# Kernel tuning notes

Measured on AMD Instinct MI355X. Metric: run time of the kernel, lower is better.

Reference implementation:

```python
import jax, jax.numpy as jnp
from jax import lax
import numpy as np

N_QUBITS = 8
Q_DEPTH = 10
DIM = 256  # 2**8

# basis-state bit table; wire 0 = most-significant bit (PennyLane convention)
_bits = ((np.arange(DIM)[:, None] >> (N_QUBITS - 1 - np.arange(N_QUBITS))) & 1)
# phase layer: S on even wires (phase i), T on odd wires (phase e^{i pi/4})
_ph = np.where(np.arange(N_QUBITS) % 2 == 0, 1j, np.exp(1j * np.pi / 4))
_diag = np.prod(np.power(_ph[None, :], _bits), axis=1)
# entangling_layer_3 CZ pattern
_cz = np.ones(DIM)
for i, j in [(0, 1), (2, 3), (4, 5), (6, 7), (1, 2), (3, 4), (5, 6)]:
    _cz = _cz * ((-1.0) ** (_bits[:, i] * _bits[:, j]))
DIAG = jnp.asarray((_diag * _cz).astype(np.complex64))  # phase+CZ layer fused diagonal
ZSIGNS = jnp.asarray((1 - 2 * _bits).astype(np.float32))  # [256, 8] PauliZ eigenvalues
H_GATE = jnp.asarray((np.array([[1.0, 1.0], [1.0, -1.0]]) / np.sqrt(2.0)).astype(np.complex64))
X_GATE = jnp.asarray(np.array([[0.0, 1.0], [1.0, 0.0]]).astype(np.complex64))
EYE2 = jnp.eye(2, dtype=jnp.complex64)
BN_EPS = 1e-5


def apply_1q(state, U, w):
    """Apply 2x2 gate U on wire w; state: [B, 2,2,...,2]."""
    state = jnp.moveaxis(state, w + 1, -1)
    state = jnp.matmul(state, U.T)
    return jnp.moveaxis(state, -1, w + 1)


def quantum_net(features, q_params):
    """Batched statevector sim of quantum_net_3. features [B,256], q_params [80] -> [B,8]."""
    f = features / jnp.linalg.norm(features, axis=1, keepdims=True)
    state = f.astype(jnp.complex64).reshape((-1,) + (2,) * N_QUBITS)
    for w in range(N_QUBITS):
        state = apply_1q(state, H_GATE, w)
    qw = q_params.reshape(Q_DEPTH, N_QUBITS)
    for layer in range(Q_DEPTH):
        for w in range(N_QUBITS):
            t = qw[layer, w]
            c = jnp.cos(t / 2).astype(jnp.complex64)
            s = jnp.sin(t / 2).astype(jnp.complex64)
            U = c * EYE2 + (-1j) * s * X_GATE  # RX(t)
            state = apply_1q(state, U, w)
        flat = state.reshape(-1, DIM) * DIAG  # phase layer + CZ entangling (diagonal)
        state = flat.reshape((-1,) + (2,) * N_QUBITS)
    sv = state.reshape(-1, DIM)
    probs = sv.real ** 2 + sv.imag ** 2
    return probs @ ZSIGNS  # [B, 8] expval(PauliZ_i)


def conv2d(x, w, b):
    y = lax.conv_general_dilated(x, w, (1, 1), 'SAME', dimension_numbers=('NCHW', 'OIHW', 'NCHW'))
    return y + b[None, :, None, None]


def bn(x, gamma, beta, mean, var):  # eval-mode BatchNorm2d
    inv = gamma / jnp.sqrt(var + BN_EPS)
    return x * inv[None, :, None, None] + (beta - mean * inv)[None, :, None, None]


def maxpool2(x):
    return lax.reduce_window(x, -jnp.inf, lax.max, (1, 1, 2, 2), (1, 1, 2, 2), 'VALID')


def setup_inputs() -> dict:
    key = jax.random.key(0)
    ks = jax.random.split(key, 16)
    B = 1024
    return {
        'x': jax.random.normal(ks[0], (B, 1, 28, 28), dtype=jnp.float32),
        'conv1_w': 0.1 * jax.random.normal(ks[1], (32, 1, 3, 3), dtype=jnp.float32),
        'conv1_b': jnp.zeros((32,), jnp.float32),
        'bn1_gamma': jnp.ones((32,), jnp.float32),
        'bn1_beta': jnp.zeros((32,), jnp.float32),
        'bn1_mean': jnp.zeros((32,), jnp.float32),
        'bn1_var': jnp.ones((32,), jnp.float32),
        'conv2_w': 0.05 * jax.random.normal(ks[2], (64, 32, 3, 3), dtype=jnp.float32),
        'conv2_b': jnp.zeros((64,), jnp.float32),
        'bn2_gamma': jnp.ones((64,), jnp.float32),
        'bn2_beta': jnp.zeros((64,), jnp.float32),
        'bn2_mean': jnp.zeros((64,), jnp.float32),
        'bn2_var': jnp.ones((64,), jnp.float32),
        'fc_w': 0.01 * jax.random.normal(ks[3], (256, 64 * 7 * 7), dtype=jnp.float32),
        'fc_b': jnp.zeros((256,), jnp.float32),
        'q_params': 0.1 * jax.random.normal(ks[4], (Q_DEPTH * N_QUBITS,), dtype=jnp.float32),
        'p1_w': 0.01 * jax.random.normal(ks[5], (128, 8), dtype=jnp.float32),
        'p1_b': jnp.zeros((128,), jnp.float32),
        'p2_w': 0.01 * jax.random.normal(ks[6], (64, 128), dtype=jnp.float32),
        'p2_b': jnp.zeros((64,), jnp.float32),
        'p3_w': 0.01 * jax.random.normal(ks[7], (10, 64), dtype=jnp.float32),
        'p3_b': jnp.zeros((10,), jnp.float32),
    }


def reference(x, conv1_w, conv1_b, bn1_gamma, bn1_beta, bn1_mean, bn1_var,
              conv2_w, conv2_b, bn2_gamma, bn2_beta, bn2_mean, bn2_var,
              fc_w, fc_b, q_params, p1_w, p1_b, p2_w, p2_b, p3_w, p3_b):
    h = maxpool2(jax.nn.relu(bn(conv2d(x, conv1_w, conv1_b), bn1_gamma, bn1_beta, bn1_mean, bn1_var)))
    h = maxpool2(jax.nn.relu(bn(conv2d(h, conv2_w, conv2_b), bn2_gamma, bn2_beta, bn2_mean, bn2_var)))
    h = h.reshape(h.shape[0], -1)  # [B, 64*7*7]
    feats = jnp.tanh(h @ fc_w.T + fc_b)  # [B, 256]
    q = quantum_net(feats, q_params)  # [B, 8]
    z = jax.nn.relu(q @ p1_w.T + p1_b)  # dropout = identity (eval)
    z = jax.nn.relu(z @ p2_w.T + p2_b)
    return z @ p3_w.T + p3_b
```

## Files before the change

### kernel.cpp

```cpp
#include <hip/hip_runtime.h>
#include <math.h>


#define B_SZ 1024

#define OFF_FCWP   0
#define OFF_W2F    802816
#define OFF_SC2    821600
#define OFF_SH2    821664
#define OFF_H1     821728
#define OFF_H2P    7244256

#define KSPLIT_FC 14
#define TS 40

typedef __attribute__((ext_vector_type(8))) short s16x8;
typedef __attribute__((ext_vector_type(4))) float f32x4;

__constant__ float C_COS8[8] = {1.f, 0.70710678f, 0.f, -0.70710678f, -1.f, -0.70710678f, 0.f, 0.70710678f};
__constant__ float C_SIN8[8] = {0.f, 0.70710678f, 1.f, 0.70710678f, 0.f, -0.70710678f, -1.f, -0.70710678f};

__device__ __forceinline__ unsigned short bf16_rne(float f) {
  unsigned u = __float_as_uint(f);
  unsigned r = u + 0x7FFFu + ((u >> 16) & 1u);
  return (unsigned short)(r >> 16);
}
__device__ __forceinline__ int div14(int m) {
  return __float2int_rz((float)m * 0.07142858f);
}

__global__ __launch_bounds__(256) void fused_front_kernel(
    const float* __restrict__ x, const float* __restrict__ c1w, const float* __restrict__ c1b,
    const float* __restrict__ bn1g, const float* __restrict__ bn1b, const float* __restrict__ bn1m,
    const float* __restrict__ bn1v,
    const float* __restrict__ c2w,
    const float* __restrict__ bn2g, const float* __restrict__ bn2b, const float* __restrict__ bn2m,
    const float* __restrict__ bn2v, const float* __restrict__ c2b,
    const float* __restrict__ fc_w,
    float* __restrict__ ws) {
  const int blk = blockIdx.x, tid = threadIdx.x;
  __shared__ float smem[3136];

  if (blk >= 1024) {
    if (blk < 1280) {
      const int n = blk - 1024;
      const float* src = fc_w + n * 3136;
      for (int i = tid; i < 3136; i += 256) smem[i] = src[i];
      __syncthreads();
      unsigned short* us = (unsigned short*)ws;
      const int nt = n >> 4, nl = n & 15;
      for (int idx = tid; idx < 784; idx += 256) {
        const int part = (idx >= 392);
        const int rest = idx - part * 392;
        const int kg = rest >> 2, q = rest & 3;
        s16x8 v;
#pragma unroll
        for (int j = 0; j < 8; ++j) {
          const int k = kg * 32 + q * 8 + j;
          float f = smem[(k & 63) * 49 + (k >> 6)];
          unsigned short hi = bf16_rne(f);
          unsigned short r = hi;
          if (part) r = bf16_rne(f - __uint_as_float((unsigned)hi << 16));
          v[j] = (short)r;
        }
        *(s16x8*)&us[((((kg * 16 + nt) * 2 + part)) << 9) + (q * 16 + nl) * 8] = v;
      }
    } else if (blk < 1424) {
      int g = (blk - 1280) * 256 + tid;
      int j = g & 7, L = (g >> 3) & 63, rest = g >> 9;
      int h = rest & 1; rest >>= 1;
      int t = rest % 9, w = rest / 9;
      int occ = w * 16 + (L & 15);
      int ic  = (L >> 4) * 8 + j;
      float v = c2w[occ * 288 + ic * 9 + t];
      unsigned short hi = bf16_rne(v);
      unsigned short res = hi;
      if (h) res = bf16_rne(v - __uint_as_float((unsigned)hi << 16));
      ((unsigned short*)(ws + OFF_W2F))[g] = res;
    } else {
      if (tid < 64) {
        float inv = bn2g[tid] / sqrtf(bn2v[tid] + 1e-5f);
        ws[OFF_SC2 + tid] = inv;
        ws[OFF_SH2 + tid] = c2b[tid] * inv + bn2b[tid] - bn2m[tid] * inv;
      }
    }
    return;
  }

  const int b = blk;
  float (*xs)[32] = (float (*)[32])smem;
  float* w1s  = smem + 960;
  float* sc1s = smem + 1248;
  float* sh1s = smem + 1280;
  float* h1 = ws + OFF_H1;

  if (tid < 240) ((float4*)smem)[tid] = make_float4(0.f, 0.f, 0.f, 0.f);
  __syncthreads();
  const float* xb = x + b * 784;
  for (int i = tid; i < 784; i += 256) {
    int y = i / 28, c = i - y * 28;
    xs[y + 1][c + 1] = xb[i];
  }
  for (int i = tid; i < 288; i += 256) w1s[i] = c1w[(i & 31) * 9 + (i >> 5)];
  if (tid < 32) {
    float inv = bn1g[tid] / sqrtf(bn1v[tid] + 1e-5f);
    sc1s[tid] = inv;
    sh1s[tid] = c1b[tid] * inv + bn1b[tid] - bn1m[tid] * inv;
  }
  __syncthreads();

  for (int t = tid; t < 448; t += 256) {
    const int oc = t & 31, py = t >> 5;
    float wv[9];
#pragma unroll
    for (int k = 0; k < 9; ++k) wv[k] = w1s[k * 32 + oc];
    float acc0[28], acc1[28];
#pragma unroll
    for (int j = 0; j < 28; ++j) { acc0[j] = 0.f; acc1[j] = 0.f; }
#pragma unroll
    for (int r = 0; r < 4; ++r) {
      const int pr = 2 * py + r;
      float row[32];
#pragma unroll
      for (int q = 0; q < 8; ++q) {
        float4 v = *(const float4*)&xs[pr][4 * q];
        row[4 * q] = v.x; row[4 * q + 1] = v.y; row[4 * q + 2] = v.z; row[4 * q + 3] = v.w;
      }
      if (r <= 2) {
#pragma unroll
        for (int kx = 0; kx < 3; ++kx) {
          const float w = wv[r * 3 + kx];
#pragma unroll
          for (int xx = 0; xx < 28; ++xx) acc0[xx] = fmaf(row[xx + kx], w, acc0[xx]);
        }
      }
      if (r >= 1) {
#pragma unroll
        for (int kx = 0; kx < 3; ++kx) {
          const float w = wv[(r - 1) * 3 + kx];
#pragma unroll
          for (int xx = 0; xx < 28; ++xx) acc1[xx] = fmaf(row[xx + kx], w, acc1[xx]);
        }
      }
    }
    const float sc = sc1s[oc], sh = sh1s[oc];
    float* dst = h1 + b * 6272 + oc * 196 + py * 14;
#pragma unroll
    for (int px = 0; px < 14; ++px) {
      float v0 = fmaxf(fmaf(acc0[2 * px], sc, sh), 0.f);
      float v1 = fmaxf(fmaf(acc0[2 * px + 1], sc, sh), 0.f);
      float v2 = fmaxf(fmaf(acc1[2 * px], sc, sh), 0.f);
      float v3 = fmaxf(fmaf(acc1[2 * px + 1], sc, sh), 0.f);
      dst[px] = fmaxf(fmaxf(v0, v1), fmaxf(v2, v3));
    }
  }
}

__global__ __launch_bounds__(256, 2) void conv2_kernel(
    const float* __restrict__ h1, const float* __restrict__ w2f_f,
    const float* __restrict__ sc2, const float* __restrict__ sh2,
    unsigned short* __restrict__ h2hi, unsigned short* __restrict__ h2lo) {
  const int b = blockIdx.x, tid = threadIdx.x;
  const int lane = tid & 63, w = tid >> 6;

  __shared__ unsigned char lds_raw[50176];
  unsigned short* tile_hi = (unsigned short*)lds_raw;
  unsigned short* tile_lo = (unsigned short*)(lds_raw + 21760);
  float* conv_out = (float*)lds_raw;

  const unsigned short* w2f = (const unsigned short*)w2f_f;
  s16x8 bf[9][2];
#pragma unroll
  for (int t = 0; t < 9; ++t)
#pragma unroll
    for (int h = 0; h < 2; ++h)
      bf[t][h] = *(const s16x8*)&w2f[(((w * 9 + t) * 2 + h) << 9) + lane * 8];

  {
    float4* z = (float4*)lds_raw;
    for (int i = tid; i < 2720; i += 256) z[i] = make_float4(0.f, 0.f, 0.f, 0.f);
  }
  __syncthreads();

  if (tid < 196) {
    const int y = div14(tid), x = tid - y * 14;
    const int sp = ((y + 1) * 16 + (x + 1)) * TS;
    const float* src = h1 + b * 6272 + tid;
#pragma unroll
    for (int c = 0; c < 4; ++c) {
      s16x8 hv, lv;
#pragma unroll
      for (int j = 0; j < 8; ++j) {
        float v = src[(c * 8 + j) * 196];
        unsigned short h16 = bf16_rne(v);
        hv[j] = (short)h16;
        lv[j] = (short)bf16_rne(v - __uint_as_float((unsigned)h16 << 16));
      }
      *(s16x8*)&tile_hi[sp + c * 8] = hv;
      *(s16x8*)&tile_lo[sp + c * 8] = lv;
    }
  }
  __syncthreads();

  f32x4 acc[13];
#pragma unroll
  for (int i = 0; i < 13; ++i) acc[i] = (f32x4){0.f, 0.f, 0.f, 0.f};

  const int kg8 = (lane >> 4) * 8;
#pragma unroll
  for (int mt = 0; mt < 13; ++mt) {
    const int m = mt * 16 + (lane & 15);
    const int y = div14(m), x = m - y * 14;
    const int base = (y * 16 + x) * TS + kg8;
#pragma unroll
    for (int dy = 0; dy < 3; ++dy) {
#pragma unroll
      for (int dx = 0; dx < 3; ++dx) {
        const int off = base + (dy * 16 + dx) * TS;
        s16x8 ah = *(s16x8*)&tile_hi[off];
        s16x8 al = *(s16x8*)&tile_lo[off];
        const int t = dy * 3 + dx;
        acc[mt] = __builtin_amdgcn_mfma_f32_16x16x32_bf16(ah, bf[t][0], acc[mt], 0, 0, 0);
        acc[mt] = __builtin_amdgcn_mfma_f32_16x16x32_bf16(ah, bf[t][1], acc[mt], 0, 0, 0);
        acc[mt] = __builtin_amdgcn_mfma_f32_16x16x32_bf16(al, bf[t][0], acc[mt], 0, 0, 0);
      }
    }
  }
  __syncthreads();

  const int oc = w * 16 + (lane & 15);
  const float sc = sc2[oc], sh = sh2[oc];
  float* cw = conv_out + w * 3136;
#pragma unroll
  for (int mt = 0; mt < 13; ++mt) {
#pragma unroll
    for (int r = 0; r < 4; ++r) {
      const int m = mt * 16 + (lane >> 4) * 4 + r;
      if (m < 196) cw[m * 16 + (lane & 15)] = fmaxf(fmaf(acc[mt][r], sc, sh), 0.f);
    }
  }
  __syncthreads();

#pragma unroll
  for (int i = 0; i < 13; ++i) {
    const int ps = i * 4 + (lane >> 4);
    if (ps < 49) {
      const int py = (ps * 37) >> 8, px = ps - py * 7;
      const int m00 = py * 28 + px * 2;
      const int c0 = m00 * 16 + (lane & 15);
      float v0 = cw[c0], v1 = cw[c0 + 16], v2 = cw[c0 + 224], v3 = cw[c0 + 240];
      float vm = fmaxf(fmaxf(v0, v1), fmaxf(v2, v3));
      unsigned short hv = bf16_rne(vm);
      const int idx = b * 3136 + ps * 64 + oc;
      h2hi[idx] = hv;
      h2lo[idx] = bf16_rne(vm - __uint_as_float((unsigned)hv << 16));
    }
  }
}

__global__ __launch_bounds__(256) void fc_mfma_kernel(
    const unsigned short* __restrict__ h2hi, const unsigned short* __restrict__ h2lo,
    const unsigned short* __restrict__ Bfrag, float* __restrict__ Part) {
  const int tid = threadIdx.x;
  const int lane = tid & 63, w = tid >> 6;
  const int nt0 = blockIdx.x * 4, z = blockIdx.z;
  const int mrow = blockIdx.y * 64 + w * 16 + (lane & 15);
  const int kg8 = (lane >> 4) * 8;
  const unsigned short* arow_hi = h2hi + mrow * 3136 + kg8;
  const unsigned short* arow_lo = h2lo + mrow * 3136 + kg8;

  f32x4 acc[4];
#pragma unroll
  for (int i = 0; i < 4; ++i) acc[i] = (f32x4){0.f, 0.f, 0.f, 0.f};

#pragma unroll
  for (int c = 0; c < 7; ++c) {
    const int kg = z * 7 + c;
    s16x8 ah = *(const s16x8*)(arow_hi + kg * 32);
    s16x8 al = *(const s16x8*)(arow_lo + kg * 32);
#pragma unroll
    for (int nf = 0; nf < 4; ++nf) {
      const unsigned short* bp = Bfrag + (size_t)((kg * 16 + nt0 + nf) * 2) * 512 + lane * 8;
      s16x8 bh = *(const s16x8*)bp;
      s16x8 bl = *(const s16x8*)(bp + 512);
      acc[nf] = __builtin_amdgcn_mfma_f32_16x16x32_bf16(ah, bh, acc[nf], 0, 0, 0);
      acc[nf] = __builtin_amdgcn_mfma_f32_16x16x32_bf16(ah, bl, acc[nf], 0, 0, 0);
      acc[nf] = __builtin_amdgcn_mfma_f32_16x16x32_bf16(al, bh, acc[nf], 0, 0, 0);
    }
  }

  float* dst = Part + (size_t)z * 262144;
  const int mbase = blockIdx.y * 64 + w * 16 + (lane >> 4) * 4;
  const int nbase = (lane & 15);
#pragma unroll
  for (int nf = 0; nf < 4; ++nf) {
#pragma unroll
    for (int r = 0; r < 4; ++r) {
      dst[(mbase + r) * 256 + (nt0 + nf) * 16 + nbase] = acc[nf][r];
    }
  }
}

__global__ __launch_bounds__(64) void quantum_kernel(
    const float* __restrict__ Part, const float* __restrict__ fc_b,
    const float* __restrict__ qp,
    const float* __restrict__ p1w, const float* __restrict__ p1b,
    const float* __restrict__ p2w, const float* __restrict__ p2b,
    const float* __restrict__ p3w, const float* __restrict__ p3b,
    float* __restrict__ out) {
  const int b = blockIdx.x, lane = threadIdx.x;
  __shared__ float csl[160];

  for (int g = lane; g < 80; g += 64) {
    float t = 0.5f * qp[g];
    csl[2 * g] = cosf(t);
    csl[2 * g + 1] = sinf(t);
  }
  __syncthreads();

  float fa[4];
#pragma unroll
  for (int a = 0; a < 4; ++a) {
    const int idx = a * 64 + lane;
    float f = fc_b[idx];
#pragma unroll
    for (int z = 0; z < KSPLIT_FC; ++z) f += Part[z * 262144 + b * 256 + idx];
    fa[a] = tanhf(f);
  }
  float ss = fa[0] * fa[0] + fa[1] * fa[1] + fa[2] * fa[2] + fa[3] * fa[3];
#pragma unroll
  for (int off = 32; off >= 1; off >>= 1) ss += __shfl_xor(ss, off);
  const float inv = 1.0f / sqrtf(ss);

  float re[4], im[4];
#pragma unroll
  for (int a = 0; a < 4; ++a) { re[a] = fa[a] * inv; im[a] = 0.f; }

  float dre[4], dim_[4];
#pragma unroll
  for (int a = 0; a < 4; ++a) {
    const int i = a * 64 + lane;
    const int k8 = (2 * __popc(i & 0xAA) + __popc(i & 0x55)) & 7;
    float dr = C_COS8[k8], di = C_SIN8[k8];
    int par = ((i >> 7) & (i >> 6)) ^ ((i >> 5) & (i >> 4)) ^ ((i >> 3) & (i >> 2)) ^ ((i >> 1) & i)
            ^ ((i >> 6) & (i >> 5)) ^ ((i >> 4) & (i >> 3)) ^ ((i >> 2) & (i >> 1));
    if (par & 1) { dr = -dr; di = -di; }
    dre[a] = dr; dim_[a] = di;
  }

  const float RS = 0.70710678118654752f;

#define H_PAIR(u, v)                                        \
  { float tur = re[u], tui = im[u];                         \
    re[u] = (tur + re[v]) * RS; im[u] = (tui + im[v]) * RS; \
    re[v] = (tur - re[v]) * RS; im[v] = (tui - im[v]) * RS; }
  H_PAIR(0, 2) H_PAIR(1, 3)
  H_PAIR(0, 1) H_PAIR(2, 3)
#pragma unroll
  for (int w = 2; w < 8; ++w) {
    const int m = 1 << (7 - w);
    const float sgn = (lane & m) ? -1.f : 1.f;
#pragma unroll
    for (int a = 0; a < 4; ++a) {
      float pre = __shfl_xor(re[a], m);
      float pim = __shfl_xor(im[a], m);
      re[a] = fmaf(sgn, re[a], pre) * RS;
      im[a] = fmaf(sgn, im[a], pim) * RS;
    }
  }

#define RX_PAIR(u, v, c, s)                                   \
  { float ur = re[u], ui = im[u], wr = re[v], wi = im[v];     \
    re[u] = fmaf(s, wi, c * ur); im[u] = fmaf(-s, wr, c * ui);\
    re[v] = fmaf(s, ui, c * wr); im[v] = fmaf(-s, ur, c * wi); }
  for (int layer = 0; layer < 10; ++layer) {
    const float* cs = &csl[16 * layer];
    { const float c = cs[0], s = cs[1]; RX_PAIR(0, 2, c, s) RX_PAIR(1, 3, c, s) }
    { const float c = cs[2], s = cs[3]; RX_PAIR(0, 1, c, s) RX_PAIR(2, 3, c, s) }
#pragma unroll
    for (int w = 2; w < 8; ++w) {
      const int m = 1 << (7 - w);
      const float c = cs[2 * w], s = cs[2 * w + 1];
#pragma unroll
      for (int a = 0; a < 4; ++a) {
        float pre = __shfl_xor(re[a], m);
        float pim = __shfl_xor(im[a], m);
        float nre = fmaf(s, pim, c * re[a]);
        float nim = fmaf(-s, pre, c * im[a]);
        if (w == 7) {
          float tre = nre * dre[a] - nim * dim_[a];
          nim = fmaf(nre, dim_[a], nim * dre[a]);
          nre = tre;
        }
        re[a] = nre; im[a] = nim;
      }
    }
  }

  float prb[4];
#pragma unroll
  for (int a = 0; a < 4; ++a) prb[a] = re[a] * re[a] + im[a] * im[a];
  float qv[8];
#pragma unroll
  for (int w = 0; w < 8; ++w) {
    float v;
    if (w == 0)      v = prb[0] + prb[1] - prb[2] - prb[3];
    else if (w == 1) v = prb[0] - prb[1] + prb[2] - prb[3];
    else {
      const int m = 1 << (7 - w);
      const float sgn = (lane & m) ? -1.f : 1.f;
      v = sgn * (prb[0] + prb[1] + prb[2] + prb[3]);
    }
#pragma unroll
    for (int off = 32; off >= 1; off >>= 1) v += __shfl_xor(v, off);
    qv[w] = v;
  }

  float z1a = p1b[lane], z1b = p1b[lane + 64];
#pragma unroll
  for (int k = 0; k < 8; ++k) {
    z1a = fmaf(qv[k], p1w[lane * 8 + k], z1a);
    z1b = fmaf(qv[k], p1w[(lane + 64) * 8 + k], z1b);
  }
  z1a = fmaxf(z1a, 0.f); z1b = fmaxf(z1b, 0.f);

  float acc2 = p2b[lane];
  const float* row2 = p2w + lane * 128;
#pragma unroll
  for (int kc = 0; kc < 64; kc += 4) {
    float4 w0 = *(const float4*)&row2[kc];
    float4 w1 = *(const float4*)&row2[64 + kc];
    float wv0[4] = {w0.x, w0.y, w0.z, w0.w};
    float wv1[4] = {w1.x, w1.y, w1.z, w1.w};
#pragma unroll
    for (int j = 0; j < 4; ++j) {
      acc2 = fmaf(__shfl(z1a, kc + j), wv0[j], acc2);
      acc2 = fmaf(__shfl(z1b, kc + j), wv1[j], acc2);
    }
  }
  const float z2 = fmaxf(acc2, 0.f);

#pragma unroll
  for (int n = 0; n < 10; ++n) {
    float p = z2 * p3w[n * 64 + lane];
#pragma unroll
    for (int off = 32; off >= 1; off >>= 1) p += __shfl_xor(p, off);
    if (lane == n) out[b * 10 + n] = p + p3b[n];
  }
}

extern "C" void kernel_launch(void* const* d_in, const int* in_sizes, int n_in,
                              void* d_out, int out_size, void* d_ws, size_t ws_size,
                              hipStream_t stream) {
  (void)in_sizes; (void)n_in; (void)out_size; (void)ws_size;
  const float* x    = (const float*)d_in[0];
  const float* c1w  = (const float*)d_in[1];
  const float* c1b  = (const float*)d_in[2];
  const float* bn1g = (const float*)d_in[3];
  const float* bn1b = (const float*)d_in[4];
  const float* bn1m = (const float*)d_in[5];
  const float* bn1v = (const float*)d_in[6];
  const float* c2w  = (const float*)d_in[7];
  const float* c2b  = (const float*)d_in[8];
  const float* bn2g = (const float*)d_in[9];
  const float* bn2b = (const float*)d_in[10];
  const float* bn2m = (const float*)d_in[11];
  const float* bn2v = (const float*)d_in[12];
  const float* fc_w = (const float*)d_in[13];
  const float* fc_b = (const float*)d_in[14];
  const float* qp   = (const float*)d_in[15];
  const float* p1w  = (const float*)d_in[16];
  const float* p1b  = (const float*)d_in[17];
  const float* p2w  = (const float*)d_in[18];
  const float* p2b  = (const float*)d_in[19];
  const float* p3w  = (const float*)d_in[20];
  const float* p3b  = (const float*)d_in[21];
  float* ws = (float*)d_ws;
  float* outp = (float*)d_out;

  unsigned short* h2hi = (unsigned short*)(ws + OFF_H2P);
  unsigned short* h2lo = h2hi + 3211264;
  const unsigned short* bfrag = (const unsigned short*)ws;

  fused_front_kernel<<<1425, 256, 0, stream>>>(x, c1w, c1b, bn1g, bn1b, bn1m, bn1v,
                                               c2w, bn2g, bn2b, bn2m, bn2v, c2b, fc_w, ws);
  conv2_kernel<<<B_SZ, 256, 0, stream>>>(ws + OFF_H1, ws + OFF_W2F, ws + OFF_SC2, ws + OFF_SH2,
                                         h2hi, h2lo);
  fc_mfma_kernel<<<dim3(4, 16, KSPLIT_FC), 256, 0, stream>>>(h2hi, h2lo, bfrag, ws + OFF_H1);
  quantum_kernel<<<B_SZ, 64, 0, stream>>>(ws + OFF_H1, fc_b, qp, p1w, p1b, p2w, p2b, p3w, p3b, outp);
}
```

Before: 179.5 us.

## Retile conv2 MFMA work as 2x2 wave grid over M and N

```diff
diff --git a/kernel.cpp b/kernel.cpp
--- a/kernel.cpp
+++ b/kernel.cpp
@@ -162,6 +162,7 @@
     unsigned short* __restrict__ h2hi, unsigned short* __restrict__ h2lo) {
   const int b = blockIdx.x, tid = threadIdx.x;
   const int lane = tid & 63, w = tid >> 6;
+  const int mh = w >> 1, nh = w & 1;
 
   __shared__ unsigned char lds_raw[50176];
   unsigned short* tile_hi = (unsigned short*)lds_raw;
@@ -169,12 +170,14 @@
   float* conv_out = (float*)lds_raw;
 
   const unsigned short* w2f = (const unsigned short*)w2f_f;
-  s16x8 bf[9][2];
+  s16x8 bf[9][2][2];
 #pragma unroll
   for (int t = 0; t < 9; ++t)
 #pragma unroll
-    for (int h = 0; h < 2; ++h)
-      bf[t][h] = *(const s16x8*)&w2f[(((w * 9 + t) * 2 + h) << 9) + lane * 8];
+    for (int ntl = 0; ntl < 2; ++ntl)
+#pragma unroll
+      for (int h = 0; h < 2; ++h)
+        bf[t][ntl][h] = *(const s16x8*)&w2f[(((((nh * 2 + ntl) * 9 + t) * 2 + h)) << 9) + lane * 8];
 
   {
     float4* z = (float4*)lds_raw;
@@ -202,53 +205,67 @@
   }
   __syncthreads();
 
-  f32x4 acc[13];
-#pragma unroll
-  for (int i = 0; i < 13; ++i) acc[i] = (f32x4){0.f, 0.f, 0.f, 0.f};
+  const int nmt = 7 - mh;
+  const int mt0 = mh * 7;
+  f32x4 acc[7][2];
+#pragma unroll
+  for (int i = 0; i < 7; ++i) { acc[i][0] = (f32x4){0,0,0,0}; acc[i][1] = (f32x4){0,0,0,0}; }
 
   const int kg8 = (lane >> 4) * 8;
 #pragma unroll
-  for (int mt = 0; mt < 13; ++mt) {
-    const int m = mt * 16 + (lane & 15);
-    const int y = div14(m), x = m - y * 14;
-    const int base = (y * 16 + x) * TS + kg8;
-#pragma unroll
-    for (int dy = 0; dy < 3; ++dy) {
-#pragma unroll
-      for (int dx = 0; dx < 3; ++dx) {
-        const int off = base + (dy * 16 + dx) * TS;
-        s16x8 ah = *(s16x8*)&tile_hi[off];
-        s16x8 al = *(s16x8*)&tile_lo[off];
-        const int t = dy * 3 + dx;
-        acc[mt] = __builtin_amdgcn_mfma_f32_16x16x32_bf16(ah, bf[t][0], acc[mt], 0, 0, 0);
-        acc[mt] = __builtin_amdgcn_mfma_f32_16x16x32_bf16(ah, bf[t][1], acc[mt], 0, 0, 0);
-        acc[mt] = __builtin_amdgcn_mfma_f32_16x16x32_bf16(al, bf[t][0], acc[mt], 0, 0, 0);
-      }
-    }
-  }
-  __syncthreads();
-
-  const int oc = w * 16 + (lane & 15);
-  const float sc = sc2[oc], sh = sh2[oc];
-  float* cw = conv_out + w * 3136;
-#pragma unroll
-  for (int mt = 0; mt < 13; ++mt) {
-#pragma unroll
-    for (int r = 0; r < 4; ++r) {
-      const int m = mt * 16 + (lane >> 4) * 4 + r;
-      if (m < 196) cw[m * 16 + (lane & 15)] = fmaxf(fmaf(acc[mt][r], sc, sh), 0.f);
-    }
-  }
-  __syncthreads();
-
+  for (int mi = 0; mi < 7; ++mi) {
+    if (mi < nmt) {
+      const int m = (mt0 + mi) * 16 + (lane & 15);
+      const int y = div14(m), x = m - y * 14;
+      const int base = (y * 16 + x) * TS + kg8;
+#pragma unroll
+      for (int dy = 0; dy < 3; ++dy) {
+#pragma unroll
+        for (int dx = 0; dx < 3; ++dx) {
+          const int off = base + (dy * 16 + dx) * TS;
+          s16x8 ah = *(s16x8*)&tile_hi[off];
+          s16x8 al = *(s16x8*)&tile_lo[off];
+          const int t = dy * 3 + dx;
+#pragma unroll
+          for (int ntl = 0; ntl < 2; ++ntl) {
+            acc[mi][ntl] = __builtin_amdgcn_mfma_f32_16x16x32_bf16(ah, bf[t][ntl][0], acc[mi][ntl], 0, 0, 0);
+            acc[mi][ntl] = __builtin_amdgcn_mfma_f32_16x16x32_bf16(ah, bf[t][ntl][1], acc[mi][ntl], 0, 0, 0);
+            acc[mi][ntl] = __builtin_amdgcn_mfma_f32_16x16x32_bf16(al, bf[t][ntl][0], acc[mi][ntl], 0, 0, 0);
+          }
+        }
+      }
+    }
+  }
+  __syncthreads();
+
+#pragma unroll
+  for (int mi = 0; mi < 7; ++mi) {
+    if (mi < nmt) {
+#pragma unroll
+      for (int ntl = 0; ntl < 2; ++ntl) {
+        const int oc = nh * 32 + ntl * 16 + (lane & 15);
+        const float sc = sc2[oc], sh = sh2[oc];
+#pragma unroll
+        for (int r = 0; r < 4; ++r) {
+          const int m = (mt0 + mi) * 16 + (lane >> 4) * 4 + r;
+          if (m < 196) conv_out[m * 64 + oc] = fmaxf(fmaf(acc[mi][ntl][r], sc, sh), 0.f);
+        }
+      }
+    }
+  }
+  __syncthreads();
+
+  const int oc = tid & 63;
 #pragma unroll
   for (int i = 0; i < 13; ++i) {
-    const int ps = i * 4 + (lane >> 4);
+    const int ps = i * 4 + (tid >> 6);
     if (ps < 49) {
       const int py = (ps * 37) >> 8, px = ps - py * 7;
       const int m00 = py * 28 + px * 2;
-      const int c0 = m00 * 16 + (lane & 15);
-      float v0 = cw[c0], v1 = cw[c0 + 16], v2 = cw[c0 + 224], v3 = cw[c0 + 240];
+      float v0 = conv_out[m00 * 64 + oc];
+      float v1 = conv_out[(m00 + 1) * 64 + oc];
+      float v2 = conv_out[(m00 + 14) * 64 + oc];
+      float v3 = conv_out[(m00 + 15) * 64 + oc];
       float vm = fmaxf(fmaxf(v0, v1), fmaxf(v2, v3));
       unsigned short hv = bf16_rne(vm);
       const int idx = b * 3136 + ps * 64 + oc;
```

Measured after the change: 179.5 us. About the same (+0.0%).
